# Kernel optimization log

Hardware: AMD Instinct MI355X
Metric: run time of the kernel (lower is better)

## Reference

```python
import jax, jax.numpy as jnp
import numpy as np


def setup_inputs() -> dict:
    key = jax.random.key(0)
    k_tok, k_lp = jax.random.split(key)
    R, S, V = 512, 1024, 50257  # rows = bsz*beam, seq_len, vocab
    tokens = jax.random.randint(k_tok, (R, S), 0, V, dtype=jnp.int64)
    lprobs = jax.random.normal(k_lp, (R, V), dtype=jnp.float32)
    return {
        "tokens": tokens,
        "lprobs": lprobs,
        "bsz": 128,
        "step": 1020,
        "beam_size": 4,
        "no_repeat_ngram_size": 3,
    }


def reference(tokens, lprobs, bsz, step, beam_size, no_repeat_ngram_size):
    # Semantics of fairseq's ngram_repeat_block CUDA kernel:
    # for each row, if tokens[row, i:i+n-1] == tokens[row, step-n+2:step+1]
    # for any window start i in [0, step-n+1], ban token tokens[row, i+n-1].
    n = no_repeat_ngram_size
    R = tokens.shape[0]
    V = lprobs.shape[1]
    num_windows = step - n + 2  # static Python int

    last = tokens[:, step - n + 2 : step + 1]            # (R, n-1) final (n-1)-gram
    starts = jnp.arange(num_windows)
    win_idx = starts[:, None] + jnp.arange(n - 1)[None, :]  # (W, n-1)
    prefixes = tokens[:, win_idx]                        # (R, W, n-1)
    match = jnp.all(prefixes == last[:, None, :], axis=-1)  # (R, W) bool
    banned = tokens[:, starts + (n - 1)]                 # (R, W) tokens to ban

    # Scatter -inf into matched banned positions; unmatched windows point
    # out-of-range (index V) and are dropped.
    scatter_idx = jnp.where(match, banned, V)            # (R, W)
    rows = jnp.arange(R)[:, None]
    return lprobs.at[rows, scatter_idx].set(-jnp.inf, mode="drop")
```

## Files before the change

### kernel.cpp

```cpp
#include <hip/hip_runtime.h>
#include <math.h>

__global__ void ngram_copy_kernel(const float4* __restrict__ in4,
                                  float4* __restrict__ out4,
                                  const float* __restrict__ in,
                                  float* __restrict__ out,
                                  long long n4, long long n_total) {
    long long i = (long long)blockIdx.x * blockDim.x + threadIdx.x;
    long long stride = (long long)gridDim.x * blockDim.x;
    for (; i < n4; i += stride) {
        out4[i] = in4[i];
    }
    if (blockIdx.x == 0 && threadIdx.x == 0) {
        for (long long t = n4 * 4; t < n_total; ++t) out[t] = in[t];
    }
}

__global__ void ngram_ban_kernel(const int* __restrict__ tokens,
                                 float* __restrict__ out,
                                 const int* __restrict__ bsz_p,
                                 const int* __restrict__ step_p,
                                 const int* __restrict__ beam_p,
                                 const int* __restrict__ n_p,
                                 long long tok_elems, long long lp_elems) {
    const int bsz  = *bsz_p;
    const int step = *step_p;
    const int beam = *beam_p;
    const int n    = *n_p;

    const int R = bsz * beam;
    const long long S = tok_elems / R;
    const long long V = lp_elems / R;
    const int num_windows = step - n + 2;
    const int last_start = step - n + 2;
    const int L = n - 1;

    for (int r = blockIdx.x; r < R; r += gridDim.x) {
        const int* __restrict__ trow = tokens + (long long)r * S;
        for (int j = threadIdx.x; j < num_windows; j += blockDim.x) {
            bool m = true;
            #pragma unroll 4
            for (int k = 0; k < L; ++k) {
                m &= (trow[j + k] == trow[last_start + k]);
            }
            if (m) {
                int banned = trow[j + n - 1];
                out[(long long)r * V + banned] = -INFINITY;
            }
        }
    }
}

extern "C" void kernel_launch(void* const* d_in, const int* in_sizes, int n_in,
                              void* d_out, int out_size, void* d_ws, size_t ws_size,
                              hipStream_t stream) {
    const int*   tokens = (const int*)d_in[0];
    const float* lprobs = (const float*)d_in[1];
    const int*   bsz_p  = (const int*)d_in[2];
    const int*   step_p = (const int*)d_in[3];
    const int*   beam_p = (const int*)d_in[4];
    const int*   n_p    = (const int*)d_in[5];
    float* out = (float*)d_out;

    const long long n_total = (long long)out_size;
    const long long n4 = n_total / 4;

    {
        const int block = 256;
        long long blocks = (n4 + block - 1) / block;
        if (blocks < 1) blocks = 1;
        if (blocks > 1048576) blocks = 1048576;
        ngram_copy_kernel<<<(int)blocks, block, 0, stream>>>(
            (const float4*)lprobs, (float4*)out, lprobs, out, n4, n_total);
    }

    {
        const int block = 256;
        const int blocks = 1024;
        ngram_ban_kernel<<<blocks, block, 0, stream>>>(
            tokens, out, bsz_p, step_p, beam_p, n_p,
            (long long)in_sizes[0], (long long)in_sizes[1]);
    }
}
```

Before: 192.9 us.

## Fuse lprobs copy and n-gram ban into one per-row kernel

```diff
diff --git a/kernel.cpp b/kernel.cpp
--- a/kernel.cpp
+++ b/kernel.cpp
@@ -1,28 +1,15 @@
 #include <hip/hip_runtime.h>
 #include <math.h>
 
-__global__ void ngram_copy_kernel(const float4* __restrict__ in4,
-                                  float4* __restrict__ out4,
-                                  const float* __restrict__ in,
-                                  float* __restrict__ out,
-                                  long long n4, long long n_total) {
-    long long i = (long long)blockIdx.x * blockDim.x + threadIdx.x;
-    long long stride = (long long)gridDim.x * blockDim.x;
-    for (; i < n4; i += stride) {
-        out4[i] = in4[i];
-    }
-    if (blockIdx.x == 0 && threadIdx.x == 0) {
-        for (long long t = n4 * 4; t < n_total; ++t) out[t] = in[t];
-    }
-}
-
-__global__ void ngram_ban_kernel(const int* __restrict__ tokens,
-                                 float* __restrict__ out,
-                                 const int* __restrict__ bsz_p,
-                                 const int* __restrict__ step_p,
-                                 const int* __restrict__ beam_p,
-                                 const int* __restrict__ n_p,
-                                 long long tok_elems, long long lp_elems) {
+__global__ void __launch_bounds__(1024)
+ngram_fused_kernel(const int* __restrict__ tokens,
+                   const float* __restrict__ lprobs,
+                   float* __restrict__ out,
+                   const int* __restrict__ bsz_p,
+                   const int* __restrict__ step_p,
+                   const int* __restrict__ beam_p,
+                   const int* __restrict__ n_p,
+                   long long tok_elems, long long lp_elems) {
     const int bsz  = *bsz_p;
     const int step = *step_p;
     const int beam = *beam_p;
@@ -31,23 +18,42 @@
     const int R = bsz * beam;
     const long long S = tok_elems / R;
     const long long V = lp_elems / R;
-    const int num_windows = step - n + 2;
-    const int last_start = step - n + 2;
-    const int L = n - 1;
+
+    const int tid = threadIdx.x;
+    const int nt  = blockDim.x;
 
     for (int r = blockIdx.x; r < R; r += gridDim.x) {
+        const long long base = (long long)r * V;
+        const long long end  = base + V;
+        const long long a    = (base + 3) & ~3LL;
+        const long long b    = end & ~3LL;
+
+        for (long long i = base + tid; i < a; i += nt) out[i] = lprobs[i];
+        {
+            const float4* __restrict__ in4  = (const float4*)(lprobs + a);
+            float4* __restrict__       out4 = (float4*)(out + a);
+            const long long nv = (b - a) >> 2;
+            #pragma unroll 4
+            for (long long i = tid; i < nv; i += nt) out4[i] = in4[i];
+        }
+        for (long long i = b + tid; i < end; i += nt) out[i] = lprobs[i];
+
+        __syncthreads();
+
+        const int num_windows = step - n + 2;
+        const int last_start  = step - n + 2;
+        const int L = n - 1;
         const int* __restrict__ trow = tokens + (long long)r * S;
-        for (int j = threadIdx.x; j < num_windows; j += blockDim.x) {
+        for (int j = tid; j < num_windows; j += nt) {
             bool m = true;
             #pragma unroll 4
-            for (int k = 0; k < L; ++k) {
-                m &= (trow[j + k] == trow[last_start + k]);
-            }
+            for (int k = 0; k < L; ++k) m &= (trow[j + k] == trow[last_start + k]);
             if (m) {
-                int banned = trow[j + n - 1];
-                out[(long long)r * V + banned] = -INFINITY;
+                const int banned = trow[j + n - 1];
+                out[base + banned] = -INFINITY;
             }
         }
+        __syncthreads();
     }
 }
 
@@ -62,23 +68,9 @@
     const int*   n_p    = (const int*)d_in[5];
     float* out = (float*)d_out;
 
-    const long long n_total = (long long)out_size;
-    const long long n4 = n_total / 4;
-
-    {
-        const int block = 256;
-        long long blocks = (n4 + block - 1) / block;
-        if (blocks < 1) blocks = 1;
-        if (blocks > 1048576) blocks = 1048576;
-        ngram_copy_kernel<<<(int)blocks, block, 0, stream>>>(
-            (const float4*)lprobs, (float4*)out, lprobs, out, n4, n_total);
-    }
-
-    {
-        const int block = 256;
-        const int blocks = 1024;
-        ngram_ban_kernel<<<blocks, block, 0, stream>>>(
-            tokens, out, bsz_p, step_p, beam_p, n_p,
-            (long long)in_sizes[0], (long long)in_sizes[1]);
-    }
+    const int blocks = 512;
+    const int block  = 1024;
+    ngram_fused_kernel<<<blocks, block, 0, stream>>>(
+        tokens, lprobs, out, bsz_p, step_p, beam_p, n_p,
+        (long long)in_sizes[0], (long long)in_sizes[1]);
 }
```

Result: slower. 200.8 us (+4.1%).
